# Performance work log

Measured on AMD Instinct MI355X. Metric: run time of the kernel, lower is better.

Reference implementation:

```python
import jax, jax.numpy as jnp
import numpy as np

N_NODES = 50000
N_EDGES = 800000
D = 128
N_GRAPHS = 128
N_CLASSES = 10
BN_EPS = 1e-5


def setup_inputs() -> dict:
    key = jax.random.key(0)
    ks = jax.random.split(key, 8)
    x = jax.random.normal(ks[0], (N_NODES, D), dtype=jnp.float32)
    edge_index = jax.random.randint(ks[1], (2, N_EDGES), 0, N_NODES, dtype=jnp.int64)
    batch = jnp.sort(jax.random.randint(ks[2], (N_NODES,), 0, N_GRAPHS, dtype=jnp.int64))
    s = 1.0 / np.sqrt(D)
    W1a = jax.random.normal(ks[3], (D, D), dtype=jnp.float32) * s
    W1b = jax.random.normal(ks[4], (D, D), dtype=jnp.float32) * s
    W2a = jax.random.normal(ks[5], (D, D), dtype=jnp.float32) * s
    W2b = jax.random.normal(ks[6], (D, D), dtype=jnp.float32) * s
    Wo = jax.random.normal(ks[7], (D, N_CLASSES), dtype=jnp.float32) * s
    z = jnp.zeros((D,), jnp.float32)
    o = jnp.ones((D,), jnp.float32)
    return dict(x=x, edge_index=edge_index, batch=batch,
                W1a=W1a, b1a=z, W1b=W1b, b1b=z, g1=o, be1=z,
                W2a=W2a, b2a=z, W2b=W2b, b2b=z, g2=o, be2=z,
                Wo=Wo, bo=jnp.zeros((N_CLASSES,), jnp.float32))


def _gin_conv(x, edge_index, Wa, ba, Wb, bb):
    # message passing: gather source features, scatter-add to targets (eps=0)
    msgs = x[edge_index[0]]                                   # [E, D]
    agg = jax.ops.segment_sum(msgs, edge_index[1], num_segments=x.shape[0])
    h = agg + x                                               # (1+eps)*x + sum_j x_j
    h = jnp.maximum(h @ Wa + ba, 0.0)                         # Linear -> ReLU
    return h @ Wb + bb                                        # Linear


def _bn_relu(h, gamma, beta):
    # BatchNorm1d (training mode: batch stats, biased var) + ReLU
    mu = jnp.mean(h, axis=0)
    var = jnp.mean(jnp.square(h - mu), axis=0)
    hn = (h - mu) * jax.lax.rsqrt(var + BN_EPS) * gamma + beta
    return jnp.maximum(hn, 0.0)


def reference(x, edge_index, batch,
              W1a, b1a, W1b, b1b, g1, be1,
              W2a, b2a, W2b, b2b, g2, be2,
              Wo, bo):
    h = _gin_conv(x, edge_index, W1a, b1a, W1b, b1b)
    h = _bn_relu(h, g1, be1)
    h = _gin_conv(h, edge_index, W2a, b2a, W2b, b2b)
    h = _bn_relu(h, g2, be2)
    pooled = jax.ops.segment_sum(h, batch, num_segments=N_GRAPHS)  # global_add_pool
    return pooled @ Wo + bo
```

## Files before the change

### kernel.cpp

```cpp
#include <hip/hip_runtime.h>

typedef __attribute__((ext_vector_type(8))) short bf16x8;
typedef __attribute__((ext_vector_type(4))) float f32x4;
typedef __attribute__((ext_vector_type(2))) float f32x2;
typedef __attribute__((ext_vector_type(2))) unsigned u32x2;

#define N_NODES 50000
#define N_EDGES 800000
#define DIM 128
#define N_GRAPHS 128
#define N_CLASSES 10
#define BN_EPS 1e-5f
#define FBLK ((N_NODES + 63) / 64)
#define NPART (FBLK * 4)
#define RED_NB 64
#define RED_ROWS ((NPART + RED_NB - 1) / RED_NB)

#define NBUCK 196
#define BCAP 32
#define FILL_NB 200
#define FILL_PER (N_EDGES / FILL_NB)
#define BMAX 6144

static __device__ __forceinline__ unsigned short f2bf(float f) {
    unsigned u = __float_as_uint(f);
    u += 0x7FFF + ((u >> 16) & 1);
    return (unsigned short)(u >> 16);
}
static __device__ __forceinline__ float bf_lo(unsigned u) { return __uint_as_float(u << 16); }
static __device__ __forceinline__ float bf_hi(unsigned u) { return __uint_as_float(u & 0xffff0000u); }
static __device__ __forceinline__ unsigned packbf(float a, float b) {
    return (unsigned)f2bf(a) | ((unsigned)f2bf(b) << 16);
}

__global__ __launch_bounds__(256) void cvt_x(const f32x2* __restrict__ x,
                                             unsigned* __restrict__ xb, int n) {
    int t = blockIdx.x * 256 + threadIdx.x;
    if (t < n) { f32x2 v = x[t]; xb[t] = packbf(v[0], v[1]); }
}

__global__ __launch_bounds__(256) void bucket_count(const int* __restrict__ ei,
                                                    int* __restrict__ gbcnt) {
    __shared__ int cnt[NBUCK];
    int tid = threadIdx.x;
    if (tid < NBUCK) cnt[tid] = 0;
    __syncthreads();
    int e0 = blockIdx.x * FILL_PER;
    for (int c = tid; c < FILL_PER; c += 256) {
        int dst = ei[N_EDGES + e0 + c];
        atomicAdd(&cnt[dst >> 8], 1);
    }
    __syncthreads();
    if (tid < NBUCK) atomicAdd(&gbcnt[tid], cnt[tid]);
}

__global__ __launch_bounds__(256) void bucket_scan(const int* __restrict__ gbcnt,
                                                   int* __restrict__ boff,
                                                   int* __restrict__ gcur) {
    __shared__ int buf[256];
    int t = threadIdx.x;
    int v = (t < NBUCK) ? gbcnt[t] : 0;
    buf[t] = v;
    __syncthreads();
#pragma unroll
    for (int off = 1; off < 256; off <<= 1) {
        int u = (t >= off) ? buf[t - off] : 0;
        __syncthreads();
        buf[t] += u;
        __syncthreads();
    }
    if (t < NBUCK) { int ex = buf[t] - v; boff[t] = ex; gcur[t] = ex; }
    if (t == 0) boff[NBUCK] = N_EDGES;
}

__global__ __launch_bounds__(256) void bucket_fill(const int* __restrict__ ei,
                                                   int* __restrict__ gcur,
                                                   unsigned* __restrict__ gbuf) {
    __shared__ unsigned bins[NBUCK * BCAP];
    __shared__ int bcnt[NBUCK];
    int tid = threadIdx.x;
    if (tid < NBUCK) bcnt[tid] = 0;
    __syncthreads();
    int e0 = blockIdx.x * FILL_PER;
    for (int c = 0; c < FILL_PER; c += 256) {
        int idx = c + tid;
        if (idx < FILL_PER) {
            int e = e0 + idx;
            int src = ei[e];
            int dst = ei[N_EDGES + e];
            int b = dst >> 8;
            unsigned w = (unsigned)src | ((unsigned)(dst & 255) << 16);
            int slot = atomicAdd(&bcnt[b], 1);
            if (slot < BCAP) bins[b * BCAP + slot] = w;
            else { int p = atomicAdd(&gcur[b], 1); gbuf[p] = w; }
        }
        __syncthreads();
        if (tid < NBUCK) {
            int cc = bcnt[tid]; if (cc > BCAP) cc = BCAP;
            int nf = cc & ~15;
            if (nf) {
                int base = atomicAdd(&gcur[tid], nf);
                for (int i = 0; i < nf; ++i) gbuf[base + i] = bins[tid * BCAP + i];
                int rem = cc - nf;
                for (int i = 0; i < rem; ++i) bins[tid * BCAP + i] = bins[tid * BCAP + nf + i];
                bcnt[tid] = rem;
            } else {
                bcnt[tid] = cc;
            }
        }
        __syncthreads();
    }
    if (tid < NBUCK) {
        int cc = bcnt[tid]; if (cc > BCAP) cc = BCAP;
        if (cc) {
            int base = atomicAdd(&gcur[tid], cc);
            for (int i = 0; i < cc; ++i) gbuf[base + i] = bins[tid * BCAP + i];
        }
    }
}

__global__ __launch_bounds__(256) void csr_build(const unsigned* __restrict__ gbuf,
                                                 const int* __restrict__ boff,
                                                 unsigned short* __restrict__ csr16,
                                                 int* __restrict__ row_start) {
    __shared__ unsigned ent[BMAX];
    __shared__ unsigned short csl[BMAX];
    __shared__ int cnt[256], c2[256], offs[256];
    int b = blockIdx.x, t = threadIdx.x;
    int base = boff[b], n = boff[b + 1] - base;
    for (int i = t; i < n; i += 256) ent[i] = gbuf[base + i];
    cnt[t] = 0; c2[t] = 0;
    __syncthreads();
    for (int i = t; i < n; i += 256) atomicAdd(&cnt[(ent[i] >> 16) & 255], 1);
    __syncthreads();
    int v = cnt[t];
    offs[t] = v;
    __syncthreads();
#pragma unroll
    for (int off = 1; off < 256; off <<= 1) {
        int u = (t >= off) ? offs[t - off] : 0;
        __syncthreads();
        offs[t] += u;
        __syncthreads();
    }
    int excl = offs[t] - v;
    int node = b * 256 + t;
    if (node < N_NODES) row_start[node] = base + excl;
    if (b == NBUCK - 1 && t == 0) row_start[N_NODES] = N_EDGES;
    __syncthreads();
    offs[t] = excl;
    __syncthreads();
    for (int i = t; i < n; i += 256) {
        unsigned w = ent[i];
        int d = (w >> 16) & 255;
        int r = atomicAdd(&c2[d], 1);
        csl[offs[d] + r] = (unsigned short)(w & 0xffffu);
    }
    __syncthreads();
    for (int i = t; i < n; i += 256) csr16[base + i] = csl[i];
}

__global__ __launch_bounds__(256) void graph_starts(const int* __restrict__ batch,
                                                    int* __restrict__ gs) {
    int g = blockIdx.x * 256 + threadIdx.x;
    if (g > N_GRAPHS) return;
    int lo = 0, hi = N_NODES;
    while (lo < hi) {
        int mid = (lo + hi) >> 1;
        if (batch[mid] < g) lo = mid + 1; else hi = mid;
    }
    gs[g] = lo;
}

template <bool BN>
__global__ __launch_bounds__(256) void aggregate_bf(const unsigned* __restrict__ F,
                                                    unsigned* __restrict__ out,
                                                    const int* __restrict__ row_start,
                                                    const unsigned short* __restrict__ csr16,
                                                    const float* __restrict__ scale,
                                                    const float* __restrict__ shift) {
    int wave = threadIdx.x >> 6, lane = threadIdx.x & 63;
    int v = blockIdx.x * 4 + wave;
    if (v >= N_NODES) return;
    float sc0 = 0.f, sc1 = 0.f, sh0 = 0.f, sh1 = 0.f;
    if (BN) {
        f32x2 s2 = ((const f32x2*)scale)[lane];
        f32x2 h2 = ((const f32x2*)shift)[lane];
        sc0 = s2[0]; sc1 = s2[1]; sh0 = h2[0]; sh1 = h2[1];
    }
    unsigned u = F[(size_t)v * 64 + lane];
    float a0 = bf_lo(u), a1 = bf_hi(u);
    if (BN) { a0 = fmaxf(a0 * sc0 + sh0, 0.f); a1 = fmaxf(a1 * sc1 + sh1, 0.f); }
    int e = row_start[v], end = row_start[v + 1];
    for (; e + 3 < end; e += 4) {
        unsigned ua = F[(size_t)csr16[e] * 64 + lane];
        unsigned ub = F[(size_t)csr16[e + 1] * 64 + lane];
        unsigned uc = F[(size_t)csr16[e + 2] * 64 + lane];
        unsigned ud = F[(size_t)csr16[e + 3] * 64 + lane];
        float p0 = bf_lo(ua), p1 = bf_hi(ua), q0 = bf_lo(ub), q1 = bf_hi(ub);
        float r0 = bf_lo(uc), r1 = bf_hi(uc), s0 = bf_lo(ud), s1 = bf_hi(ud);
        if (BN) {
            p0 = fmaxf(p0 * sc0 + sh0, 0.f); p1 = fmaxf(p1 * sc1 + sh1, 0.f);
            q0 = fmaxf(q0 * sc0 + sh0, 0.f); q1 = fmaxf(q1 * sc1 + sh1, 0.f);
            r0 = fmaxf(r0 * sc0 + sh0, 0.f); r1 = fmaxf(r1 * sc1 + sh1, 0.f);
            s0 = fmaxf(s0 * sc0 + sh0, 0.f); s1 = fmaxf(s1 * sc1 + sh1, 0.f);
        }
        a0 += (p0 + q0) + (r0 + s0);
        a1 += (p1 + q1) + (r1 + s1);
    }
    for (; e < end; ++e) {
        unsigned ua = F[(size_t)csr16[e] * 64 + lane];
        float p0 = bf_lo(ua), p1 = bf_hi(ua);
        if (BN) { p0 = fmaxf(p0 * sc0 + sh0, 0.f); p1 = fmaxf(p1 * sc1 + sh1, 0.f); }
        a0 += p0; a1 += p1;
    }
    out[(size_t)v * 64 + lane] = packbf(a0, a1);
}

__global__ __launch_bounds__(256) void prep_w(const float* __restrict__ W0,
                                              const float* __restrict__ W1,
                                              const float* __restrict__ W2,
                                              const float* __restrict__ W3,
                                              unsigned short* __restrict__ wf) {
    int t = blockIdx.x * 256 + threadIdx.x;
    if (t >= 4 * 16384) return;
    int m = t >> 14, rem = t & 16383;
    int e = rem & 7, lane = (rem >> 3) & 63, fi = rem >> 9;
    int ks = fi & 3, n = fi >> 2;
    int col = n * 16 + (lane & 15);
    int k = ks * 32 + ((lane >> 4) << 3) + e;
    const float* W = (m == 0) ? W0 : (m == 1) ? W1 : (m == 2) ? W2 : W3;
    wf[t] = f2bf(W[k * DIM + col]);
}

__global__ __launch_bounds__(256, 3) void fused_layer(
        const unsigned short* __restrict__ A,
        const bf16x8* __restrict__ wfA_g,
        const bf16x8* __restrict__ wfB_g,
        const float* __restrict__ bias_a,
        const float* __restrict__ bias_b,
        unsigned short* __restrict__ out,
        float* __restrict__ psum,
        float* __restrict__ psq, int M) {
    __shared__ bf16x8 wfS[2048];
    __shared__ unsigned short mid[8192];

    int tid = threadIdx.x;
    int w = tid >> 6, lane = tid & 63;
    int cl = lane & 15, kq = lane >> 4;
    int rblk = blockIdx.x * 64;

    bf16x8 wb[8];
#pragma unroll
    for (int i = 0; i < 8; ++i) wb[i] = wfB_g[i * 256 + tid];

#pragma unroll
    for (int i = 0; i < 8; ++i) wfS[i * 256 + tid] = wfA_g[i * 256 + tid];

    int arow = rblk + w * 16 + cl;
    if (arow >= M) arow = M - 1;
    bf16x8 af[4];
    const unsigned short* Ap = A + (size_t)arow * DIM + kq * 8;
#pragma unroll
    for (int ks = 0; ks < 4; ++ks) af[ks] = *(const bf16x8*)(Ap + ks * 32);

    __syncthreads();

    f32x4 acc[8];
#pragma unroll
    for (int n = 0; n < 8; ++n) acc[n] = f32x4{0.f, 0.f, 0.f, 0.f};
#pragma unroll
    for (int n = 0; n < 8; ++n)
#pragma unroll
        for (int ks = 0; ks < 4; ++ks)
            acc[n] = __builtin_amdgcn_mfma_f32_16x16x32_bf16(af[ks], wfS[(n * 4 + ks) * 64 + lane],
                                                             acc[n], 0, 0, 0);

#pragma unroll
    for (int n = 0; n < 8; ++n) {
        int col = n * 16 + cl;
        float b = bias_a[col];
#pragma unroll
        for (int r = 0; r < 4; ++r) {
            int rl = w * 16 + kq * 4 + r;
            float v = fmaxf(acc[n][r] + b, 0.f);
            mid[(rl * DIM + col) ^ ((rl & 7) << 3)] = f2bf(v);
        }
    }
    __syncthreads();

#pragma unroll
    for (int i = 0; i < 8; ++i) wfS[i * 256 + tid] = wb[i];

    bf16x8 af2[4];
    {
        int rl = w * 16 + cl;
        int sw = (cl & 7) << 3;
#pragma unroll
        for (int ks = 0; ks < 4; ++ks)
            af2[ks] = *(const bf16x8*)(mid + ((rl * DIM + kq * 8 + ks * 32) ^ sw));
    }
    __syncthreads();

    f32x4 acc2[8];
#pragma unroll
    for (int n = 0; n < 8; ++n) acc2[n] = f32x4{0.f, 0.f, 0.f, 0.f};
#pragma unroll
    for (int n = 0; n < 8; ++n)
#pragma unroll
        for (int ks = 0; ks < 4; ++ks)
            acc2[n] = __builtin_amdgcn_mfma_f32_16x16x32_bf16(af2[ks], wfS[(n * 4 + ks) * 64 + lane],
                                                              acc2[n], 0, 0, 0);

    int prow = blockIdx.x * 4 + w;
#pragma unroll
    for (int n = 0; n < 8; ++n) {
        int col = n * 16 + cl;
        float b = bias_b[col];
        float s = 0.f, q = 0.f;
#pragma unroll
        for (int r = 0; r < 4; ++r) {
            int rl = w * 16 + kq * 4 + r;
            float v = acc2[n][r] + b;
            if (rblk + rl < M) { s += v; q += v * v; }
            mid[(rl * DIM + col) ^ ((rl & 7) << 3)] = f2bf(v);
        }
        s += __shfl_xor(s, 16, 64);
        s += __shfl_xor(s, 32, 64);
        q += __shfl_xor(q, 16, 64);
        q += __shfl_xor(q, 32, 64);
        if (kq == 0) {
            psum[(size_t)prow * DIM + col] = s;
            psq[(size_t)prow * DIM + col] = q;
        }
    }

    {
        int r4 = lane >> 4, c = lane & 15;
#pragma unroll
        for (int rb = 0; rb < 4; ++rb) {
            int rl = w * 16 + rb * 4 + r4;
            int grow = rblk + rl;
            bf16x8 v = *(const bf16x8*)(mid + ((rl * DIM + c * 8) ^ ((rl & 7) << 3)));
            if (grow < M) *(bf16x8*)(out + (size_t)grow * DIM + c * 8) = v;
        }
    }
}

__global__ __launch_bounds__(256) void reduce_stats(const float* __restrict__ psum,
                                                    const float* __restrict__ psq,
                                                    float* __restrict__ ps2) {
    int b = blockIdx.x, t = threadIdx.x;
    int c = t & 127;
    const float* src = (t < 128) ? psum : psq;
    int r0 = b * RED_ROWS;
    int r1 = min(NPART, r0 + RED_ROWS);
    float acc = 0.f;
    for (int r = r0; r < r1; ++r) acc += src[(size_t)r * DIM + c];
    ps2[(size_t)b * 256 + t] = acc;
}

__global__ __launch_bounds__(256) void bn_finalize(const float* __restrict__ ps2,
                                                   const float* __restrict__ g,
                                                   const float* __restrict__ be,
                                                   float* __restrict__ scale,
                                                   float* __restrict__ shift) {
    __shared__ float sums[128], sqs[128];
    int t = threadIdx.x;
    int c = t & 127;
    float acc = 0.f;
#pragma unroll 4
    for (int r = 0; r < RED_NB; ++r) acc += ps2[(size_t)r * 256 + t];
    if (t < 128) sums[c] = acc; else sqs[c] = acc;
    __syncthreads();
    if (t < 128) {
        const float invN = 1.0f / (float)N_NODES;
        float mu = sums[c] * invN;
        float var = sqs[c] * invN - mu * mu;
        float rs = rsqrtf(var + BN_EPS) * g[c];
        scale[c] = rs;
        shift[c] = be[c] - mu * rs;
    }
}

__global__ __launch_bounds__(256) void bn_pool(const unsigned short* __restrict__ h,
                                               const float* __restrict__ scale,
                                               const float* __restrict__ shift,
                                               const int* __restrict__ gs,
                                               float* __restrict__ pooled) {
    int g = blockIdx.x;
    int t = threadIdx.x;
    int c4 = t & 31;
    int rs = t >> 5;
    int r0 = gs[g], r1 = gs[g + 1];
    f32x4 sc = ((const f32x4*)scale)[c4];
    f32x4 sh = ((const f32x4*)shift)[c4];
    f32x4 acc = f32x4{0.f, 0.f, 0.f, 0.f};
    for (int r = r0 + rs; r < r1; r += 8) {
        u32x2 u = *(const u32x2*)(h + (size_t)r * DIM + c4 * 4);
        float f0 = bf_lo(u[0]), f1 = bf_hi(u[0]), f2 = bf_lo(u[1]), f3 = bf_hi(u[1]);
        acc[0] += fmaxf(f0 * sc[0] + sh[0], 0.f);
        acc[1] += fmaxf(f1 * sc[1] + sh[1], 0.f);
        acc[2] += fmaxf(f2 * sc[2] + sh[2], 0.f);
        acc[3] += fmaxf(f3 * sc[3] + sh[3], 0.f);
    }
    __shared__ f32x4 red[256];
    red[t] = acc;
    __syncthreads();
#pragma unroll
    for (int off = 128; off >= 32; off >>= 1) {
        if (t < off) red[t] += red[t + off];
        __syncthreads();
    }
    if (t < 32) ((f32x4*)pooled)[g * 32 + c4] = red[t];
}

__global__ __launch_bounds__(256) void final_gemm(const float* __restrict__ pooled,
                                                  const float* __restrict__ Wo,
                                                  const float* __restrict__ bo,
                                                  float* __restrict__ out) {
    int t = blockIdx.x * 256 + threadIdx.x;
    if (t >= N_GRAPHS * N_CLASSES) return;
    int g = t / N_CLASSES, c = t - g * N_CLASSES;
    float s = bo[c];
    const float* p = pooled + (size_t)g * DIM;
#pragma unroll 4
    for (int k = 0; k < DIM; ++k) s += p[k] * Wo[k * N_CLASSES + c];
    out[t] = s;
}

extern "C" void kernel_launch(void* const* d_in, const int* in_sizes, int n_in,
                              void* d_out, int out_size, void* d_ws, size_t ws_size,
                              hipStream_t stream) {
    const float* x   = (const float*)d_in[0];
    const int* ei    = (const int*)d_in[1];
    const int* batch = (const int*)d_in[2];
    const float* W1a = (const float*)d_in[3];
    const float* b1a = (const float*)d_in[4];
    const float* W1b = (const float*)d_in[5];
    const float* b1b = (const float*)d_in[6];
    const float* g1  = (const float*)d_in[7];
    const float* be1 = (const float*)d_in[8];
    const float* W2a = (const float*)d_in[9];
    const float* b2a = (const float*)d_in[10];
    const float* W2b = (const float*)d_in[11];
    const float* b2b = (const float*)d_in[12];
    const float* g2  = (const float*)d_in[13];
    const float* be2 = (const float*)d_in[14];
    const float* Wo  = (const float*)d_in[15];
    const float* bo  = (const float*)d_in[16];

    char* ws = (char*)d_ws;
    const size_t NBH = (size_t)N_NODES * DIM * 2;
    unsigned short* xb   = (unsigned short*)ws;
    unsigned short* aggb = (unsigned short*)(ws + NBH);
    unsigned short* hb   = (unsigned short*)(ws + 2 * NBH);
    unsigned short* wfrag = (unsigned short*)(ws + 3 * NBH);
    float* psum = (float*)(ws + 3 * NBH + 4 * 16384 * 2);
    float* psq  = psum + (size_t)NPART * DIM;
    float* ps2  = psq + (size_t)NPART * DIM;
    float* pooled  = ps2 + RED_NB * 256;
    float* scale1  = pooled + N_GRAPHS * DIM;
    float* shift1  = scale1 + 128;
    float* scale2  = scale1 + 256;
    float* shift2  = scale1 + 384;
    int* gs        = (int*)(shift2 + 128);
    int* gbcnt     = gs + N_GRAPHS + 1;
    int* boff      = gbcnt + NBUCK;
    int* gcur      = boff + NBUCK + 1;
    int* row_start = gcur + NBUCK;
    unsigned* gbuf = (unsigned*)(row_start + N_NODES + 1);
    unsigned short* csr16 = (unsigned short*)(gbuf + N_EDGES);

    hipMemsetAsync(gbcnt, 0, NBUCK * 4, stream);

    const int nv2 = N_NODES * 64;
    cvt_x<<<(nv2 + 255) / 256, 256, 0, stream>>>((const f32x2*)x, (unsigned*)xb, nv2);
    prep_w<<<256, 256, 0, stream>>>(W1a, W1b, W2a, W2b, wfrag);
    graph_starts<<<1, 256, 0, stream>>>(batch, gs);

    bucket_count<<<FILL_NB, 256, 0, stream>>>(ei, gbcnt);
    bucket_scan<<<1, 256, 0, stream>>>(gbcnt, boff, gcur);
    bucket_fill<<<FILL_NB, 256, 0, stream>>>(ei, gcur, gbuf);
    csr_build<<<NBUCK, 256, 0, stream>>>(gbuf, boff, csr16, row_start);

    const int ablk = (N_NODES + 3) / 4;

    aggregate_bf<false><<<ablk, 256, 0, stream>>>((const unsigned*)xb, (unsigned*)aggb,
                                                  row_start, csr16, nullptr, nullptr);
    fused_layer<<<FBLK, 256, 0, stream>>>(
        aggb, (const bf16x8*)(wfrag + 0 * 16384), (const bf16x8*)(wfrag + 1 * 16384),
        b1a, b1b, hb, psum, psq, N_NODES);
    reduce_stats<<<RED_NB, 256, 0, stream>>>(psum, psq, ps2);
    bn_finalize<<<1, 256, 0, stream>>>(ps2, g1, be1, scale1, shift1);

    aggregate_bf<true><<<ablk, 256, 0, stream>>>((const unsigned*)hb, (unsigned*)aggb,
                                                 row_start, csr16, scale1, shift1);
    fused_layer<<<FBLK, 256, 0, stream>>>(
        aggb, (const bf16x8*)(wfrag + 2 * 16384), (const bf16x8*)(wfrag + 3 * 16384),
        b2a, b2b, hb, psum, psq, N_NODES);
    reduce_stats<<<RED_NB, 256, 0, stream>>>(psum, psq, ps2);
    bn_finalize<<<1, 256, 0, stream>>>(ps2, g2, be2, scale2, shift2);
    bn_pool<<<N_GRAPHS, 256, 0, stream>>>(hb, scale2, shift2, gs, pooled);

    final_gemm<<<(N_GRAPHS * N_CLASSES + 255) / 256, 256, 0, stream>>>(pooled, Wo, bo,
                                                                       (float*)d_out);
}
```

Measured before the change: 272.4 us.

## Replace per-bucket LDS bins with block-local counting sort in bucket_fill

Each bucket_fill block now loads its whole edge chunk into LDS and histograms the destination buckets. It then does a prefix scan and reserves one global range per bucket with a single atomic, scatters the edges into sorted order in LDS, and writes them out as contiguous runs. This replaces the old scheme of 16-entry flushes with global atomic overflow and serial per-thread copy loops, which cost many synchronisations and strided single-thread writes. It also doubles the block count so each block handles 2000 edges, which uses about 16KB of LDS for the two staging arrays.

```diff
diff --git a/kernel.cpp b/kernel.cpp
--- a/kernel.cpp
+++ b/kernel.cpp
@@ -17,8 +17,7 @@
 #define RED_ROWS ((NPART + RED_NB - 1) / RED_NB)
 
 #define NBUCK 196
-#define BCAP 32
-#define FILL_NB 200
+#define FILL_NB 400
 #define FILL_PER (N_EDGES / FILL_NB)
 #define BMAX 6144
 
@@ -76,46 +75,45 @@
 __global__ __launch_bounds__(256) void bucket_fill(const int* __restrict__ ei,
                                                    int* __restrict__ gcur,
                                                    unsigned* __restrict__ gbuf) {
-    __shared__ unsigned bins[NBUCK * BCAP];
-    __shared__ int bcnt[NBUCK];
+    __shared__ unsigned ent[FILL_PER];
+    __shared__ unsigned srt[FILL_PER];
+    __shared__ int cnt[256], c2[256], lofs[256], gbase[256];
     int tid = threadIdx.x;
-    if (tid < NBUCK) bcnt[tid] = 0;
-    __syncthreads();
     int e0 = blockIdx.x * FILL_PER;
-    for (int c = 0; c < FILL_PER; c += 256) {
-        int idx = c + tid;
-        if (idx < FILL_PER) {
-            int e = e0 + idx;
-            int src = ei[e];
-            int dst = ei[N_EDGES + e];
-            int b = dst >> 8;
-            unsigned w = (unsigned)src | ((unsigned)(dst & 255) << 16);
-            int slot = atomicAdd(&bcnt[b], 1);
-            if (slot < BCAP) bins[b * BCAP + slot] = w;
-            else { int p = atomicAdd(&gcur[b], 1); gbuf[p] = w; }
-        }
-        __syncthreads();
-        if (tid < NBUCK) {
-            int cc = bcnt[tid]; if (cc > BCAP) cc = BCAP;
-            int nf = cc & ~15;
-            if (nf) {
-                int base = atomicAdd(&gcur[tid], nf);
-                for (int i = 0; i < nf; ++i) gbuf[base + i] = bins[tid * BCAP + i];
-                int rem = cc - nf;
-                for (int i = 0; i < rem; ++i) bins[tid * BCAP + i] = bins[tid * BCAP + nf + i];
-                bcnt[tid] = rem;
-            } else {
-                bcnt[tid] = cc;
-            }
-        }
-        __syncthreads();
-    }
-    if (tid < NBUCK) {
-        int cc = bcnt[tid]; if (cc > BCAP) cc = BCAP;
-        if (cc) {
-            int base = atomicAdd(&gcur[tid], cc);
-            for (int i = 0; i < cc; ++i) gbuf[base + i] = bins[tid * BCAP + i];
-        }
+    cnt[tid] = 0; c2[tid] = 0;
+    __syncthreads();
+    for (int i = tid; i < FILL_PER; i += 256) {
+        int src = ei[e0 + i];
+        int dst = ei[N_EDGES + e0 + i];
+        ent[i] = (unsigned)src | ((unsigned)(dst & 255) << 16) | ((unsigned)(dst >> 8) << 24);
+        atomicAdd(&cnt[dst >> 8], 1);
+    }
+    __syncthreads();
+    int v = cnt[tid];
+    lofs[tid] = v;
+    __syncthreads();
+#pragma unroll
+    for (int off = 1; off < 256; off <<= 1) {
+        int u = (tid >= off) ? lofs[tid - off] : 0;
+        __syncthreads();
+        lofs[tid] += u;
+        __syncthreads();
+    }
+    int excl = lofs[tid] - v;
+    lofs[tid] = excl;
+    if (tid < NBUCK && v > 0) gbase[tid] = atomicAdd(&gcur[tid], v);
+    __syncthreads();
+    for (int i = tid; i < FILL_PER; i += 256) {
+        unsigned w = ent[i];
+        int b = w >> 24;
+        int r = atomicAdd(&c2[b], 1);
+        srt[lofs[b] + r] = w;
+    }
+    __syncthreads();
+    for (int i = tid; i < FILL_PER; i += 256) {
+        unsigned w = srt[i];
+        int b = w >> 24;
+        gbuf[gbase[b] + (i - lofs[b])] = w;
     }
 }
 
```

New measurement: 251.6 us. 7.6% less time.
